# Kernel tuning notes

Hardware: AMD Instinct MI355X
Metric: run time of the kernel (lower is better)

Reference implementation:

```python
import jax, jax.numpy as jnp
import numpy as np

DIM = 512
NUM_LATENTS = 128
TRUE_BATCH = 8
DOWNSCALING = 16


def setup_inputs() -> dict:
    key = jax.random.key(0)
    ks = jax.random.split(key, 7)
    B = TRUE_BATCH * NUM_LATENTS
    s = 0.02
    return {
        "x": jax.random.normal(ks[0], (B, DOWNSCALING, DIM), dtype=jnp.float32),
        "l": jax.random.normal(ks[1], (B, NUM_LATENTS, DIM), dtype=jnp.float32),
        "Wq": jax.random.normal(ks[2], (DIM, DIM), dtype=jnp.float32) * s,
        "Wk": jax.random.normal(ks[3], (DIM, DIM), dtype=jnp.float32) * s,
        "Wv": jax.random.normal(ks[4], (DIM, DIM), dtype=jnp.float32) * s,
        "Wo": jax.random.normal(ks[5], (DIM, DIM), dtype=jnp.float32) * s,
        "bo": jax.random.normal(ks[6], (DIM,), dtype=jnp.float32) * s,
        "num_heads": 8,
    }


def reference(x, l, Wq, Wk, Wv, Wo, bo, num_heads):
    B, n_tok, d = x.shape
    num_latents = l.shape[1]
    dh = d // num_heads

    def split_heads(t):
        # (b, n, h*d) -> (b, h, n, d)
        b, n, _ = t.shape
        return t.reshape(b, n, num_heads, dh).transpose(0, 2, 1, 3)

    q = split_heads(x @ Wq.T)   # (B, h, n_tok, dh)
    k = split_heads(l @ Wk.T)   # (B, h, num_latents, dh)
    v = split_heads(l @ Wv.T)

    scores = jnp.einsum('bhid,bhjd->bhij', q, k) * (dh ** -0.5)

    # mask row for batch element b is row (b mod num_latents) of a causal triu mask:
    # latent index m may attend only to latents j <= m.
    row = jnp.arange(B) % num_latents                       # (B,)
    allowed = jnp.arange(num_latents)[None, :] <= row[:, None]  # (B, num_latents)
    mask = jnp.where(allowed, 0.0, -jnp.inf).astype(scores.dtype)

    scores = scores + mask[:, None, None, :]
    attn = jax.nn.softmax(scores, axis=-1)

    out = jnp.einsum('bhij,bhjd->bhid', attn, v)            # (B, h, n_tok, dh)
    out = out.transpose(0, 2, 1, 3).reshape(B, n_tok, d)
    return out @ Wo.T + bo
```

## Files before the change

kernel.cpp:

```cpp
#include <hip/hip_runtime.h>


typedef __bf16 bf16;
typedef __attribute__((ext_vector_type(8))) __bf16 bf16x8;
typedef __attribute__((ext_vector_type(4))) __bf16 bf16x4;
typedef __attribute__((ext_vector_type(4))) float  float4v;

#define MFMA16(a, b, c) __builtin_amdgcn_mfma_f32_16x16x32_bf16((a), (b), (c), 0, 0, 0)

__device__ __forceinline__ void gl2lds16(const bf16* g, bf16* l) {
    __builtin_amdgcn_global_load_lds(
        (const __attribute__((address_space(1))) void*)g,
        (__attribute__((address_space(3))) void*)l, 16, 0, 0);
}

__global__ __launch_bounds__(256) void cast_f32_bf16(const float* __restrict__ src,
                                                     bf16* __restrict__ dst, int n4) {
    const int stride = gridDim.x * 256;
    for (int i = blockIdx.x * 256 + threadIdx.x; i < n4; i += stride) {
        float4v f = ((const float4v*)src)[i];
        ((bf16x4*)dst)[i] = bf16x4{(bf16)f.x, (bf16)f.y, (bf16)f.z, (bf16)f.w};
    }
}

__global__ __launch_bounds__(256) void cast_weights(const float* __restrict__ Wq,
                                                    const float* __restrict__ Wk,
                                                    const float* __restrict__ Wv,
                                                    const float* __restrict__ Wo,
                                                    bf16* __restrict__ Wq_b,
                                                    bf16* __restrict__ Wkv_b,
                                                    bf16* __restrict__ Wo_b) {
    const int i = blockIdx.x * 256 + threadIdx.x;
    const int w = i >> 16;
    const int j = i & 65535;
    const float* src = (w == 0) ? Wq : (w == 1) ? Wk : (w == 2) ? Wv : Wo;
    bf16x4* dst = (w == 0) ? (bf16x4*)Wq_b
                : (w == 1) ? (bf16x4*)Wkv_b
                : (w == 2) ? ((bf16x4*)Wkv_b) + 65536
                           : (bf16x4*)Wo_b;
    float4v f = ((const float4v*)src)[j];
    dst[j] = bf16x4{(bf16)f.x, (bf16)f.y, (bf16)f.z, (bf16)f.w};
}

template <bool FOUT>
__global__ __launch_bounds__(256) void gemm_bt(const bf16* __restrict__ A,
                                               const bf16* __restrict__ W,
                                               void* __restrict__ Cp,
                                               const float* __restrict__ bias,
                                               int ldC) {
    __shared__ alignas(16) bf16 Asl[128 * 32];
    __shared__ alignas(16) bf16 Bsl[128 * 32];

    const int tid  = threadIdx.x;
    const int n0   = blockIdx.x * 128;
    const int m0   = blockIdx.y * 128;

    const int wave = tid >> 6;
    const int lane = tid & 63;
    const int mi   = lane & 15;
    const int quad = lane >> 4;
    const int qrow = (wave >> 1) * 64;
    const int qcol = (wave & 1) * 64;

    const int srow = wave * 16 + (lane >> 2);
    const int scol = (lane & 3) * 8;

    float4v acc[4][4] = {};

    for (int kt = 0; kt < 16; ++kt) {
        const int k0 = kt * 32;
#pragma unroll
        for (int r = 0; r < 2; ++r) {
            gl2lds16(A + (size_t)(m0 + srow + r * 64) * 512 + k0 + scol,
                     &Asl[wave * 512 + r * 2048]);
            gl2lds16(W + (size_t)(n0 + srow + r * 64) * 512 + k0 + scol,
                     &Bsl[wave * 512 + r * 2048]);
        }
        __syncthreads();

        bf16x8 af[4], bfr[4];
#pragma unroll
        for (int i = 0; i < 4; ++i)
            af[i] = *(const bf16x8*)&Asl[(qrow + i * 16 + mi) * 32 + quad * 8];
#pragma unroll
        for (int j = 0; j < 4; ++j)
            bfr[j] = *(const bf16x8*)&Bsl[(qcol + j * 16 + mi) * 32 + quad * 8];
#pragma unroll
        for (int i = 0; i < 4; ++i)
#pragma unroll
            for (int j = 0; j < 4; ++j)
                acc[i][j] = MFMA16(af[i], bfr[j], acc[i][j]);
        __syncthreads();
    }

#pragma unroll
    for (int i = 0; i < 4; ++i) {
#pragma unroll
        for (int j = 0; j < 4; ++j) {
            const int row = m0 + qrow + i * 16 + quad * 4;
            const int col = n0 + qcol + j * 16 + mi;
#pragma unroll
            for (int r = 0; r < 4; ++r) {
                float v = acc[i][j][r];
                if (FOUT)
                    ((float*)Cp)[(size_t)(row + r) * ldC + col] = v + bias[col];
                else
                    ((bf16*)Cp)[(size_t)(row + r) * ldC + col] = (bf16)v;
            }
        }
    }
}

__global__ __launch_bounds__(64) void attn_kernel(const bf16* __restrict__ Q,
                                                  const bf16* __restrict__ KV,
                                                  bf16* __restrict__ O) {
    __shared__ alignas(16) bf16 Plds[16 * 136];

    const int bh     = blockIdx.x;
    const int b      = bh >> 3;
    const int h      = bh & 7;
    const int rowb   = b & 127;
    const int ntiles = (rowb >> 4) + 1;
    const int nkt    = (ntiles + 1) >> 1;
    const int lane   = threadIdx.x;
    const int mi     = lane & 15;
    const int quad   = lane >> 4;

    const bf16* qbase = Q + (size_t)(b * 16 + mi) * 512 + h * 64 + quad * 8;
    const bf16x8 aq0 = *(const bf16x8*)(qbase);
    const bf16x8 aq1 = *(const bf16x8*)(qbase + 32);

    float4v sc[8];
    const bf16* kbase = KV + (size_t)(b * 128 + mi) * 1024 + h * 64 + quad * 8;
#pragma unroll
    for (int jt = 0; jt < 8; ++jt) {
        if (jt < ntiles) {
            const bf16* kb = kbase + (size_t)jt * 16 * 1024;
            bf16x8 bk0 = *(const bf16x8*)(kb);
            bf16x8 bk1 = *(const bf16x8*)(kb + 32);
            float4v a = {};
            a = MFMA16(aq0, bk0, a);
            a = MFMA16(aq1, bk1, a);
            sc[jt] = a;
        }
    }

#pragma unroll
    for (int jt = 0; jt < 8; ++jt) {
        if (jt < ntiles) {
            const bool masked = (jt * 16 + mi) > rowb;
#pragma unroll
            for (int r = 0; r < 4; ++r)
                sc[jt][r] = masked ? -1e30f : sc[jt][r] * 0.125f;
        }
    }

#pragma unroll
    for (int r = 0; r < 4; ++r) {
        float mx = sc[0][r];
#pragma unroll
        for (int jt = 1; jt < 8; ++jt)
            if (jt < ntiles) mx = fmaxf(mx, sc[jt][r]);
#pragma unroll
        for (int off = 1; off < 16; off <<= 1) mx = fmaxf(mx, __shfl_xor(mx, off, 64));
        float s = 0.f;
#pragma unroll
        for (int jt = 0; jt < 8; ++jt) {
            if (jt < ntiles) {
                float p = __expf(sc[jt][r] - mx);
                sc[jt][r] = p;
                s += p;
            }
        }
#pragma unroll
        for (int off = 1; off < 16; off <<= 1) s += __shfl_xor(s, off, 64);
        const float inv = 1.f / s;
#pragma unroll
        for (int jt = 0; jt < 8; ++jt) {
            if (jt < 2 * nkt) {
                float p = (jt < ntiles) ? sc[jt][r] * inv : 0.f;
                Plds[(quad * 4 + r) * 136 + jt * 16 + mi] = (bf16)p;
            }
        }
    }
    __syncthreads();

    float4v ao[4] = {};
#pragma unroll
    for (int ks = 0; ks < 4; ++ks) {
        if (ks < nkt) {
            bf16x8 ap = *(const bf16x8*)&Plds[mi * 136 + ks * 32 + quad * 8];
            const bf16* vbase = KV + (size_t)(b * 128 + ks * 32 + quad * 8) * 1024
                               + 512 + h * 64;
#pragma unroll
            for (int jt = 0; jt < 4; ++jt) {
                bf16x8 bv;
#pragma unroll
                for (int j = 0; j < 8; ++j)
                    bv[j] = vbase[(size_t)j * 1024 + jt * 16 + mi];
                ao[jt] = MFMA16(ap, bv, ao[jt]);
            }
        }
    }

#pragma unroll
    for (int jt = 0; jt < 4; ++jt)
#pragma unroll
        for (int r = 0; r < 4; ++r)
            O[(size_t)(b * 16 + quad * 4 + r) * 512 + h * 64 + jt * 16 + mi] =
                (bf16)ao[jt][r];
}

extern "C" void kernel_launch(void* const* d_in, const int* in_sizes, int n_in,
                              void* d_out, int out_size, void* d_ws, size_t ws_size,
                              hipStream_t stream) {
    const float* x  = (const float*)d_in[0];
    const float* l  = (const float*)d_in[1];
    const float* Wq = (const float*)d_in[2];
    const float* Wk = (const float*)d_in[3];
    const float* Wv = (const float*)d_in[4];
    const float* Wo = (const float*)d_in[5];
    const float* bo = (const float*)d_in[6];

    char* ws = (char*)d_ws;
    size_t off = 0;
    bf16* Wq_b  = (bf16*)(ws + off); off += (size_t)512 * 512 * 2;
    bf16* Wo_b  = (bf16*)(ws + off); off += (size_t)512 * 512 * 2;
    bf16* Wkv_b = (bf16*)(ws + off); off += (size_t)1024 * 512 * 2;
    bf16* xb    = (bf16*)(ws + off); off += (size_t)16384 * 512 * 2;
    bf16* lb    = (bf16*)(ws + off); off += (size_t)131072 * 512 * 2;
    bf16* Qb    = (bf16*)(ws + off); off += (size_t)16384 * 512 * 2;
    bf16* KVb   = (bf16*)(ws + off); off += (size_t)131072 * 1024 * 2;
    bf16* AOb   = (bf16*)(ws + off);

    cast_weights<<<1024, 256, 0, stream>>>(Wq, Wk, Wv, Wo, Wq_b, Wkv_b, Wo_b);
    cast_f32_bf16<<<2048, 256, 0, stream>>>(x, xb, 16384 * 512 / 4);
    cast_f32_bf16<<<8192, 256, 0, stream>>>(l, lb, 131072 * 512 / 4);

    gemm_bt<false><<<dim3(4, 128),  256, 0, stream>>>(xb, Wq_b,  Qb,  nullptr, 512);
    gemm_bt<false><<<dim3(8, 1024), 256, 0, stream>>>(lb, Wkv_b, KVb, nullptr, 1024);

    attn_kernel<<<8192, 64, 0, stream>>>(Qb, KVb, AOb);

    gemm_bt<true><<<dim3(4, 128), 256, 0, stream>>>(AOb, Wo_b, d_out, bo, 512);
}
```

Measured before the change: 730.3 us.

## Write V transposed from KV GEMM, pack attention waves, XCD-aware tile mapping

The KV projection GEMM now writes K row-major into its own buffer and V transposed per batch/dim (latent-contiguous). This lets the attention kernel load V fragments as 16-byte vectors instead of eight strided scalar loads. The attention kernel packs four (batch,head) waves per 256-thread block, each with its own LDS slice. GEMM blocks use a 1D grid remapped so that consecutive M tiles land on the same XCD, which is meant to improve L2 reuse of A rows. The transposed V store is scattered with bf16x4 writes, which may cost some write efficiency.

```diff
diff --git a/kernel.cpp b/kernel.cpp
--- a/kernel.cpp
+++ b/kernel.cpp
@@ -42,19 +42,25 @@
     dst[j] = bf16x4{(bf16)f.x, (bf16)f.y, (bf16)f.z, (bf16)f.w};
 }
 
-template <bool FOUT>
+template <int MODE>
 __global__ __launch_bounds__(256) void gemm_bt(const bf16* __restrict__ A,
                                                const bf16* __restrict__ W,
-                                               void* __restrict__ Cp,
+                                               void* __restrict__ C0,
+                                               void* __restrict__ C1,
                                                const float* __restrict__ bias,
-                                               int ldC) {
+                                               int nT, int mPerXcd) {
     __shared__ alignas(16) bf16 Asl[128 * 32];
     __shared__ alignas(16) bf16 Bsl[128 * 32];
 
+    const int bid = blockIdx.x;
+    const int xcd = bid & 7;
+    const int s   = bid >> 3;
+    const int mt  = xcd * mPerXcd + s / nT;
+    const int nt  = s % nT;
+    const int m0  = mt * 128;
+    const int n0  = nt * 128;
+
     const int tid  = threadIdx.x;
-    const int n0   = blockIdx.x * 128;
-    const int m0   = blockIdx.y * 128;
-
     const int wave = tid >> 6;
     const int lane = tid & 63;
     const int mi   = lane & 15;
@@ -93,6 +99,21 @@
         __syncthreads();
     }
 
+    if (MODE == 1 && nt >= 4) {
+        const size_t b = (size_t)mt;
+#pragma unroll
+        for (int i = 0; i < 4; ++i) {
+            const int lat0 = qrow + i * 16 + quad * 4;
+#pragma unroll
+            for (int j = 0; j < 4; ++j) {
+                const int dd = (n0 - 512) + qcol + j * 16 + mi;
+                bf16x4 o = {(bf16)acc[i][j][0], (bf16)acc[i][j][1],
+                            (bf16)acc[i][j][2], (bf16)acc[i][j][3]};
+                *(bf16x4*)((bf16*)C1 + (b * 512 + dd) * 128 + lat0) = o;
+            }
+        }
+        return;
+    }
 #pragma unroll
     for (int i = 0; i < 4; ++i) {
 #pragma unroll
@@ -102,27 +123,29 @@
 #pragma unroll
             for (int r = 0; r < 4; ++r) {
                 float v = acc[i][j][r];
-                if (FOUT)
-                    ((float*)Cp)[(size_t)(row + r) * ldC + col] = v + bias[col];
+                if (MODE == 2)
+                    ((float*)C0)[(size_t)(row + r) * 512 + col] = v + bias[col];
                 else
-                    ((bf16*)Cp)[(size_t)(row + r) * ldC + col] = (bf16)v;
-            }
-        }
-    }
-}
-
-__global__ __launch_bounds__(64) void attn_kernel(const bf16* __restrict__ Q,
-                                                  const bf16* __restrict__ KV,
-                                                  bf16* __restrict__ O) {
-    __shared__ alignas(16) bf16 Plds[16 * 136];
-
-    const int bh     = blockIdx.x;
+                    ((bf16*)C0)[(size_t)(row + r) * 512 + col] = (bf16)v;
+            }
+        }
+    }
+}
+
+__global__ __launch_bounds__(256) void attn_kernel(const bf16* __restrict__ Q,
+                                                   const bf16* __restrict__ K,
+                                                   const bf16* __restrict__ Vt,
+                                                   bf16* __restrict__ O) {
+    __shared__ alignas(16) bf16 Plds[4][16 * 136];
+
+    const int w      = threadIdx.x >> 6;
+    const int bh     = blockIdx.x * 4 + w;
     const int b      = bh >> 3;
     const int h      = bh & 7;
     const int rowb   = b & 127;
     const int ntiles = (rowb >> 4) + 1;
     const int nkt    = (ntiles + 1) >> 1;
-    const int lane   = threadIdx.x;
+    const int lane   = threadIdx.x & 63;
     const int mi     = lane & 15;
     const int quad   = lane >> 4;
 
@@ -131,11 +154,11 @@
     const bf16x8 aq1 = *(const bf16x8*)(qbase + 32);
 
     float4v sc[8];
-    const bf16* kbase = KV + (size_t)(b * 128 + mi) * 1024 + h * 64 + quad * 8;
+    const bf16* kbase = K + (size_t)(b * 128 + mi) * 512 + h * 64 + quad * 8;
 #pragma unroll
     for (int jt = 0; jt < 8; ++jt) {
         if (jt < ntiles) {
-            const bf16* kb = kbase + (size_t)jt * 16 * 1024;
+            const bf16* kb = kbase + (size_t)jt * 16 * 512;
             bf16x8 bk0 = *(const bf16x8*)(kb);
             bf16x8 bk1 = *(const bf16x8*)(kb + 32);
             float4v a = {};
@@ -179,25 +202,22 @@
         for (int jt = 0; jt < 8; ++jt) {
             if (jt < 2 * nkt) {
                 float p = (jt < ntiles) ? sc[jt][r] * inv : 0.f;
-                Plds[(quad * 4 + r) * 136 + jt * 16 + mi] = (bf16)p;
+                Plds[w][(quad * 4 + r) * 136 + jt * 16 + mi] = (bf16)p;
             }
         }
     }
     __syncthreads();
 
     float4v ao[4] = {};
+    const bf16* vb0 = Vt + ((size_t)b * 512 + h * 64) * 128;
 #pragma unroll
     for (int ks = 0; ks < 4; ++ks) {
         if (ks < nkt) {
-            bf16x8 ap = *(const bf16x8*)&Plds[mi * 136 + ks * 32 + quad * 8];
-            const bf16* vbase = KV + (size_t)(b * 128 + ks * 32 + quad * 8) * 1024
-                               + 512 + h * 64;
+            bf16x8 ap = *(const bf16x8*)&Plds[w][mi * 136 + ks * 32 + quad * 8];
 #pragma unroll
             for (int jt = 0; jt < 4; ++jt) {
-                bf16x8 bv;
-#pragma unroll
-                for (int j = 0; j < 8; ++j)
-                    bv[j] = vbase[(size_t)j * 1024 + jt * 16 + mi];
+                bf16x8 bv = *(const bf16x8*)(vb0 + (size_t)(jt * 16 + mi) * 128
+                                             + ks * 32 + quad * 8);
                 ao[jt] = MFMA16(ap, bv, ao[jt]);
             }
         }
@@ -230,17 +250,18 @@
     bf16* xb    = (bf16*)(ws + off); off += (size_t)16384 * 512 * 2;
     bf16* lb    = (bf16*)(ws + off); off += (size_t)131072 * 512 * 2;
     bf16* Qb    = (bf16*)(ws + off); off += (size_t)16384 * 512 * 2;
-    bf16* KVb   = (bf16*)(ws + off); off += (size_t)131072 * 1024 * 2;
+    bf16* Kb    = (bf16*)(ws + off); off += (size_t)131072 * 512 * 2;
+    bf16* Vtb   = (bf16*)(ws + off); off += (size_t)1024 * 512 * 128 * 2;
     bf16* AOb   = (bf16*)(ws + off);
 
     cast_weights<<<1024, 256, 0, stream>>>(Wq, Wk, Wv, Wo, Wq_b, Wkv_b, Wo_b);
     cast_f32_bf16<<<2048, 256, 0, stream>>>(x, xb, 16384 * 512 / 4);
     cast_f32_bf16<<<8192, 256, 0, stream>>>(l, lb, 131072 * 512 / 4);
 
-    gemm_bt<false><<<dim3(4, 128),  256, 0, stream>>>(xb, Wq_b,  Qb,  nullptr, 512);
-    gemm_bt<false><<<dim3(8, 1024), 256, 0, stream>>>(lb, Wkv_b, KVb, nullptr, 1024);
-
-    attn_kernel<<<8192, 64, 0, stream>>>(Qb, KVb, AOb);
-
-    gemm_bt<true><<<dim3(4, 128), 256, 0, stream>>>(AOb, Wo_b, d_out, bo, 512);
-}
+    gemm_bt<0><<<512,  256, 0, stream>>>(xb, Wq_b,  Qb, nullptr, nullptr, 4, 16);
+    gemm_bt<1><<<8192, 256, 0, stream>>>(lb, Wkv_b, Kb, Vtb,     nullptr, 8, 128);
+
+    attn_kernel<<<2048, 256, 0, stream>>>(Qb, Kb, Vtb, AOb);
+
+    gemm_bt<2><<<512, 256, 0, stream>>>(AOb, Wo_b, d_out, nullptr, bo, 4, 16);
+}
```

Result: faster. 714.6 us (-2.2%).
